# Kernel tuning notes

Measured on AMD Instinct MI355X. Metric: run time of the kernel, lower is better.

## Reference

```python
import jax, jax.numpy as jnp
import numpy as np

UNITS = 256
NUM_HEADS = 8
HEAD_DIM = UNITS // NUM_HEADS
B, N = 8, 2048


def setup_inputs() -> dict:
    key = jax.random.key(0)
    ks = jax.random.split(key, 7)
    node_features = jax.random.normal(ks[0], (B, N, UNITS), dtype=jnp.float32)
    adjacency_matrix = jax.random.randint(ks[1], (B, N, N), 0, 2, dtype=jnp.int32)
    # Glorot-ish scaled dense weights
    s = 1.0 / np.sqrt(UNITS)
    Wq = jax.random.normal(ks[2], (UNITS, UNITS), dtype=jnp.float32) * s
    Wk = jax.random.normal(ks[3], (UNITS, UNITS), dtype=jnp.float32) * s
    Wv = jax.random.normal(ks[4], (UNITS, UNITS), dtype=jnp.float32) * s
    Wo = jax.random.normal(ks[5], (UNITS, UNITS), dtype=jnp.float32) * s
    bo = jnp.zeros((UNITS,), dtype=jnp.float32)
    return {"node_features": node_features, "adjacency_matrix": adjacency_matrix,
            "Wq": Wq, "Wk": Wk, "Wv": Wv, "Wo": Wo, "bo": bo}


def reference(node_features, adjacency_matrix, Wq, Wk, Wv, Wo, bo):
    b, n, _ = node_features.shape
    h, d = NUM_HEADS, HEAD_DIM
    # projections -> [b, h, n, d]
    q = (node_features @ Wq).reshape(b, n, h, d).transpose(0, 2, 1, 3)
    k = (node_features @ Wk).reshape(b, n, h, d).transpose(0, 2, 1, 3)
    v = (node_features @ Wv).reshape(b, n, h, d).transpose(0, 2, 1, 3)
    scores = jnp.einsum('bhqd,bhkd->bhqk', q, k) / jnp.sqrt(jnp.float32(d))
    mask = adjacency_matrix[:, None, :, :] > 0  # [b,1,n,n] broadcasts over heads
    scores = jnp.where(mask, scores, jnp.float32(-1e9))
    w = jax.nn.softmax(scores, axis=-1)
    # dropout is identity at inference (training=None)
    ctx = jnp.einsum('bhqk,bhkd->bhqd', w, v)
    ctx = ctx.transpose(0, 2, 1, 3).reshape(b, n, h * d)
    return ctx @ Wo + bo
```

## Files before the change

kernel.cpp:

```cpp
#include <hip/hip_runtime.h>
#include <cstdint>
#include <cstddef>

#define B_ 8
#define N_ 2048
#define H_ 8
#define D_ 32
#define U_ 256

typedef _Float16 half8 __attribute__((ext_vector_type(8)));
typedef _Float16 half4 __attribute__((ext_vector_type(4)));
typedef float float4v __attribute__((ext_vector_type(4)));

__device__ __forceinline__ float fast_exp2(float x) {
#if __has_builtin(__builtin_amdgcn_exp2f)
  return __builtin_amdgcn_exp2f(x);
#else
  return exp2f(x);
#endif
}

__global__ __launch_bounds__(256, 2)
void k_qkv(const float* __restrict__ X,
           const float* __restrict__ Wq, const float* __restrict__ Wk,
           const float* __restrict__ Wv,
           _Float16* __restrict__ Qg, _Float16* __restrict__ Kg,
           _Float16* __restrict__ VTg)
{
  __shared__ __attribute__((aligned(16))) char qsmem[36864];
  _Float16* Xs = (_Float16*)qsmem;
  _Float16* Ws = (_Float16*)(qsmem + 18432);

  const int tid  = threadIdx.x;
  const int lane = tid & 63;
  const int w    = tid >> 6;
  const int c    = lane & 15;
  const int qd   = lane >> 4;

  const int bx   = blockIdx.x;
  const int proj = bx >> 1;
  const int nh   = bx & 1;
  const int n0l  = nh * 128;
  const int m0   = blockIdx.y * 128;
  const float* Wp = (proj == 0) ? Wq : ((proj == 1) ? Wk : Wv);
  const float wscale = (proj == 0) ? 0.25505413f : 1.0f;

  const float4v zero4 = {0.f, 0.f, 0.f, 0.f};
  float4v acc[2][8];
#pragma unroll
  for (int i = 0; i < 2; ++i)
#pragma unroll
    for (int j = 0; j < 8; ++j) acc[i][j] = zero4;

  for (int kt = 0; kt < 4; ++kt) {
    const int k0 = kt * 64;
    {
      const int row = tid >> 1;
      const int off = (tid & 1) * 32;
      const float* src = X + (size_t)(m0 + row) * U_ + k0 + off;
      _Float16* dst = &Xs[row * 72 + off];
#pragma unroll
      for (int i = 0; i < 4; ++i) {
        float4v a  = *(const float4v*)(src + i * 8);
        float4v b2 = *(const float4v*)(src + i * 8 + 4);
        half8 hv;
        hv[0] = (_Float16)a[0];  hv[1] = (_Float16)a[1];
        hv[2] = (_Float16)a[2];  hv[3] = (_Float16)a[3];
        hv[4] = (_Float16)b2[0]; hv[5] = (_Float16)b2[1];
        hv[6] = (_Float16)b2[2]; hv[7] = (_Float16)b2[3];
        *(half8*)(dst + i * 8) = hv;
      }
    }
    {
      const int kl = tid & 63;
      const int ng = tid >> 6;
      const float* srcw = Wp + (size_t)(k0 + kl) * U_ + n0l + ng * 32;
#pragma unroll
      for (int j = 0; j < 8; ++j) {
        float4v a = *(const float4v*)(srcw + j * 4);
#pragma unroll
        for (int jj = 0; jj < 4; ++jj)
          Ws[(ng * 32 + j * 4 + jj) * 72 + kl] = (_Float16)(a[jj] * wscale);
      }
    }
    __syncthreads();
#pragma unroll
    for (int ks = 0; ks < 2; ++ks) {
      half8 af[2], bf[8];
#pragma unroll
      for (int mt = 0; mt < 2; ++mt)
        af[mt] = *(const half8*)&Xs[(w * 32 + mt * 16 + c) * 72 + ks * 32 + qd * 8];
#pragma unroll
      for (int nt = 0; nt < 8; ++nt)
        bf[nt] = *(const half8*)&Ws[(nt * 16 + c) * 72 + ks * 32 + qd * 8];
#pragma unroll
      for (int mt = 0; mt < 2; ++mt)
#pragma unroll
        for (int nt = 0; nt < 8; ++nt)
          acc[mt][nt] = __builtin_amdgcn_mfma_f32_16x16x32_f16(af[mt], bf[nt], acc[mt][nt], 0, 0, 0);
    }
    __syncthreads();
  }

  const int b   = m0 >> 11;
  const int nb0 = m0 & (N_ - 1);
  if (proj < 2) {
    _Float16* Og = (proj == 0) ? Qg : Kg;
#pragma unroll
    for (int mt = 0; mt < 2; ++mt)
#pragma unroll
      for (int nt = 0; nt < 8; ++nt)
#pragma unroll
        for (int r = 0; r < 4; ++r) {
          const int rowl = w * 32 + mt * 16 + qd * 4 + r;
          Og[(size_t)(b * N_ + nb0 + rowl) * U_ + n0l + nt * 16 + c] = (_Float16)acc[mt][nt][r];
        }
  } else {
    _Float16* tr = (_Float16*)qsmem;
#pragma unroll
    for (int mt = 0; mt < 2; ++mt)
#pragma unroll
      for (int nt = 0; nt < 8; ++nt)
#pragma unroll
        for (int r = 0; r < 4; ++r)
          tr[(nt * 16 + c) * 136 + w * 32 + mt * 16 + qd * 4 + r] = (_Float16)acc[mt][nt][r];
    __syncthreads();
    const int u = tid >> 1;
    const int seg = tid & 1;
    _Float16* dst = VTg + (size_t)(b * U_ + n0l + u) * N_ + nb0 + seg * 64;
#pragma unroll
    for (int i = 0; i < 8; ++i)
      *(half8*)(dst + i * 8) = *(const half8*)&tr[u * 136 + seg * 64 + i * 8];
  }
}

#define KS_H (32 * 264)
#define VT_H (256 * 40)

struct StageRegs {
  half8 k0, k1, v0, v1;
  int a0, a1, a2, a3;
};

__global__ __launch_bounds__(512, 2)
void k_attn(const _Float16* __restrict__ Qg, const _Float16* __restrict__ Kg,
            const _Float16* __restrict__ VTg, const int* __restrict__ Adj,
            _Float16* __restrict__ Cg)
{
  __shared__ __attribute__((aligned(16))) _Float16 KsB[2][KS_H];
  __shared__ __attribute__((aligned(16))) _Float16 VTsB[2][VT_H];
  __shared__ __attribute__((aligned(8)))  unsigned int maskB[2][64];

  const int tid  = threadIdx.x;
  const int lane = tid & 63;
  const int w    = tid >> 6;
  const int c    = lane & 15;
  const int qd   = lane >> 4;
  const int wg   = blockIdx.x;
  const int b    = wg & 7;
  const int q0   = (wg >> 3) * 64;

  const _Float16* kptr = Kg + (size_t)(b * N_ + (tid >> 4)) * U_ + (tid & 15) * 16;
  const _Float16* vptr = VTg + (size_t)(b * U_ + (tid >> 1)) * N_ + (tid & 1) * 16;
  const int rr = lane >> 5;
  const int kk = lane & 31;
  const int* aptr = Adj + (size_t)(b * N_ + q0 + w * 8 + rr) * N_ + kk;

  half8 qb[4];
#pragma unroll
  for (int nt = 0; nt < 4; ++nt)
    qb[nt] = *(const half8*)(Qg + (size_t)(b * N_ + q0 + nt * 16 + c) * U_ + w * D_ + qd * 8);

  const float4v init4 = {-8.f, -8.f, -8.f, -8.f};
  const float4v zero4 = {0.f, 0.f, 0.f, 0.f};
  float4v acc[2][4];
#pragma unroll
  for (int i = 0; i < 2; ++i)
#pragma unroll
    for (int j = 0; j < 4; ++j) acc[i][j] = zero4;
  float lrow[4] = {0.f, 0.f, 0.f, 0.f};

  auto load_tile = [&](int kt) -> StageRegs {
    StageRegs r;
    const _Float16* ks = kptr + (size_t)kt * 32 * U_;
    const _Float16* vs = vptr + (size_t)kt * 32;
    const int* as = aptr + (size_t)kt * 32;
    r.k0 = *(const half8*)ks;  r.k1 = *(const half8*)(ks + 8);
    r.v0 = *(const half8*)vs;  r.v1 = *(const half8*)(vs + 8);
    r.a0 = as[0];
    r.a1 = as[2 * N_];
    r.a2 = as[4 * N_];
    r.a3 = as[6 * N_];
    return r;
  };
  auto store_tile = [&](const StageRegs& r, int buf) {
    _Float16* kd = &KsB[buf][(tid >> 4) * 264 + (tid & 15) * 16];
    *(half8*)kd = r.k0;  *(half8*)(kd + 8) = r.k1;
    _Float16* vd = &VTsB[buf][(tid >> 1) * 40 + (tid & 1) * 16];
    *(half8*)vd = r.v0;  *(half8*)(vd + 8) = r.v1;
    unsigned long long bm;
    bm = __ballot(r.a0 > 0); if (lane == 0) *(unsigned long long*)&maskB[buf][w * 8 + 0] = bm;
    bm = __ballot(r.a1 > 0); if (lane == 0) *(unsigned long long*)&maskB[buf][w * 8 + 2] = bm;
    bm = __ballot(r.a2 > 0); if (lane == 0) *(unsigned long long*)&maskB[buf][w * 8 + 4] = bm;
    bm = __ballot(r.a3 > 0); if (lane == 0) *(unsigned long long*)&maskB[buf][w * 8 + 6] = bm;
  };
  auto compute_tile = [&](int buf) {
    half8 ka0 = *(const half8*)&KsB[buf][(0 * 16 + c) * 264 + w * D_ + qd * 8];
    half8 ka1 = *(const half8*)&KsB[buf][(1 * 16 + c) * 264 + w * D_ + qd * 8];
    half4 va[2][2];
#pragma unroll
    for (int mt = 0; mt < 2; ++mt)
#pragma unroll
      for (int kc = 0; kc < 2; ++kc)
        va[mt][kc] = *(const half4*)&VTsB[buf][(w * D_ + mt * 16 + c) * 40 + kc * 16 + qd * 4];
#pragma unroll
    for (int nt = 0; nt < 4; ++nt) {
      float4v s0 = __builtin_amdgcn_mfma_f32_16x16x32_f16(ka0, qb[nt], init4, 0, 0, 0);
      float4v s1 = __builtin_amdgcn_mfma_f32_16x16x32_f16(ka1, qb[nt], init4, 0, 0, 0);
      const unsigned int mq = maskB[buf][nt * 16 + c];
      const unsigned int t0 = mq >> (qd * 4);
      const unsigned int t1 = mq >> (16 + qd * 4);
      half4 pb0, pb1;
      float ls = 0.f;
#pragma unroll
      for (int r = 0; r < 4; ++r) {
        float e0 = fast_exp2(s0[r]);
        float e1 = fast_exp2(s1[r]);
        float p0 = ((t0 >> r) & 1u) ? e0 : 0.f;
        float p1 = ((t1 >> r) & 1u) ? e1 : 0.f;
        ls += p0 + p1;
        pb0[r] = (_Float16)p0;
        pb1[r] = (_Float16)p1;
      }
      lrow[nt] += ls;
      acc[0][nt] = __builtin_amdgcn_mfma_f32_16x16x16f16(va[0][0], pb0, acc[0][nt], 0, 0, 0);
      acc[0][nt] = __builtin_amdgcn_mfma_f32_16x16x16f16(va[0][1], pb1, acc[0][nt], 0, 0, 0);
      acc[1][nt] = __builtin_amdgcn_mfma_f32_16x16x16f16(va[1][0], pb0, acc[1][nt], 0, 0, 0);
      acc[1][nt] = __builtin_amdgcn_mfma_f32_16x16x16f16(va[1][1], pb1, acc[1][nt], 0, 0, 0);
    }
  };

  {
    StageRegs r = load_tile(0);
    store_tile(r, 0);
  }
  __syncthreads();

#pragma unroll 1
  for (int kt = 0; kt < 64; kt += 2) {
    {
      StageRegs r = load_tile(kt + 1);
      compute_tile(0);
      store_tile(r, 1);
    }
    __syncthreads();
    if (kt + 2 < 64) {
      StageRegs r = load_tile(kt + 2);
      compute_tile(1);
      store_tile(r, 0);
    } else {
      compute_tile(1);
    }
    __syncthreads();
  }

  float rinv[4];
#pragma unroll
  for (int nt = 0; nt < 4; ++nt) {
    float l = lrow[nt];
    l += __shfl_xor(l, 16, 64);
    l += __shfl_xor(l, 32, 64);
    rinv[nt] = (l > 0.f) ? 1.f / l : 0.f;
  }
  _Float16* ctxS = (_Float16*)KsB;
#pragma unroll
  for (int mt = 0; mt < 2; ++mt)
#pragma unroll
    for (int nt = 0; nt < 4; ++nt) {
      half4 hv;
#pragma unroll
      for (int r = 0; r < 4; ++r)
        hv[r] = (_Float16)(acc[mt][nt][r] * rinv[nt]);
      *(half4*)&ctxS[(nt * 16 + c) * 264 + w * D_ + mt * 16 + qd * 4] = hv;
    }
  __syncthreads();
  {
    const int row = tid >> 3;
    const int seg = tid & 7;
    _Float16* dst = Cg + (size_t)(b * N_ + q0 + row) * U_ + seg * 32;
#pragma unroll
    for (int i = 0; i < 4; ++i)
      *(half8*)(dst + i * 8) = *(const half8*)&ctxS[row * 264 + seg * 32 + i * 8];
  }
}

__global__ __launch_bounds__(256, 2)
void k_out(const _Float16* __restrict__ Cg, const float* __restrict__ Wo,
           const float* __restrict__ bo, float* __restrict__ Out)
{
  __shared__ __attribute__((aligned(16))) char osmem[36864];
  _Float16* Xs = (_Float16*)osmem;
  _Float16* Ws = (_Float16*)(osmem + 18432);

  const int tid  = threadIdx.x;
  const int lane = tid & 63;
  const int w    = tid >> 6;
  const int c    = lane & 15;
  const int qd   = lane >> 4;
  const int n0l  = blockIdx.x * 128;
  const int m0   = blockIdx.y * 128;

  const float4v zero4 = {0.f, 0.f, 0.f, 0.f};
  float4v acc[2][8];
#pragma unroll
  for (int i = 0; i < 2; ++i)
#pragma unroll
    for (int j = 0; j < 8; ++j) acc[i][j] = zero4;

  for (int kt = 0; kt < 4; ++kt) {
    const int k0 = kt * 64;
    {
      const int row = tid >> 1;
      const int off = (tid & 1) * 32;
      const _Float16* src = Cg + (size_t)(m0 + row) * U_ + k0 + off;
      _Float16* dst = &Xs[row * 72 + off];
#pragma unroll
      for (int i = 0; i < 4; ++i)
        *(half8*)(dst + i * 8) = *(const half8*)(src + i * 8);
    }
    {
      const int kl = tid & 63;
      const int ng = tid >> 6;
      const float* srcw = Wo + (size_t)(k0 + kl) * U_ + n0l + ng * 32;
#pragma unroll
      for (int j = 0; j < 8; ++j) {
        float4v a = *(const float4v*)(srcw + j * 4);
#pragma unroll
        for (int jj = 0; jj < 4; ++jj)
          Ws[(ng * 32 + j * 4 + jj) * 72 + kl] = (_Float16)a[jj];
      }
    }
    __syncthreads();
#pragma unroll
    for (int ks = 0; ks < 2; ++ks) {
      half8 af[2], bf[8];
#pragma unroll
      for (int mt = 0; mt < 2; ++mt)
        af[mt] = *(const half8*)&Xs[(w * 32 + mt * 16 + c) * 72 + ks * 32 + qd * 8];
#pragma unroll
      for (int nt = 0; nt < 8; ++nt)
        bf[nt] = *(const half8*)&Ws[(nt * 16 + c) * 72 + ks * 32 + qd * 8];
#pragma unroll
      for (int mt = 0; mt < 2; ++mt)
#pragma unroll
        for (int nt = 0; nt < 8; ++nt)
          acc[mt][nt] = __builtin_amdgcn_mfma_f32_16x16x32_f16(af[mt], bf[nt], acc[mt][nt], 0, 0, 0);
    }
    __syncthreads();
  }

#pragma unroll
  for (int nt = 0; nt < 8; ++nt) {
    const float bias = bo[n0l + nt * 16 + c];
#pragma unroll
    for (int mt = 0; mt < 2; ++mt)
#pragma unroll
      for (int r = 0; r < 4; ++r) {
        const int rowl = w * 32 + mt * 16 + qd * 4 + r;
        Out[(size_t)(m0 + rowl) * U_ + n0l + nt * 16 + c] = acc[mt][nt][r] + bias;
      }
  }
}

extern "C" void kernel_launch(void* const* d_in, const int* in_sizes, int n_in,
                              void* d_out, int out_size, void* d_ws, size_t ws_size,
                              hipStream_t stream) {
  const float* X   = (const float*)d_in[0];
  const int*   Adj = (const int*)d_in[1];
  const float* Wq  = (const float*)d_in[2];
  const float* Wk  = (const float*)d_in[3];
  const float* Wv  = (const float*)d_in[4];
  const float* Wo  = (const float*)d_in[5];
  const float* bo  = (const float*)d_in[6];
  float* Out = (float*)d_out;

  const size_t elems = (size_t)B_ * N_ * U_;
  _Float16* Qg  = (_Float16*)d_ws;
  _Float16* Kg  = Qg + elems;
  _Float16* VTg = Kg + elems;
  _Float16* Cg  = VTg + elems;

  k_qkv<<<dim3(6, 128), 256, 0, stream>>>(X, Wq, Wk, Wv, Qg, Kg, VTg);
  k_attn<<<dim3(256), 512, 0, stream>>>(Qg, Kg, VTg, Adj, Cg);
  k_out<<<dim3(2, 128), 256, 0, stream>>>(Cg, Wo, bo, Out);
}
```

Baseline: 351.8 us.

## Prepack fp16 inputs/weights, drop LDS staging in GEMMs, halve attention query tile

```diff
diff --git a/kernel.cpp b/kernel.cpp
--- a/kernel.cpp
+++ b/kernel.cpp
@@ -20,30 +20,76 @@
 #endif
 }
 
+__global__ __launch_bounds__(256)
+void k_prep(const float* __restrict__ X,
+            const float* __restrict__ Wq, const float* __restrict__ Wk,
+            const float* __restrict__ Wv, const float* __restrict__ Wo,
+            _Float16* __restrict__ Xh, _Float16* __restrict__ WT)
+{
+  const int bid = blockIdx.x, tid = threadIdx.x;
+  if (bid < 512) {
+    const size_t base = ((size_t)bid * 256 + tid) * 32;
+    const float* src = X + base;
+    _Float16* dst = Xh + base;
+#pragma unroll
+    for (int i = 0; i < 4; ++i) {
+      float4v a = *(const float4v*)(src + i * 8);
+      float4v b = *(const float4v*)(src + i * 8 + 4);
+      half8 h;
+      h[0] = (_Float16)a[0]; h[1] = (_Float16)a[1];
+      h[2] = (_Float16)a[2]; h[3] = (_Float16)a[3];
+      h[4] = (_Float16)b[0]; h[5] = (_Float16)b[1];
+      h[6] = (_Float16)b[2]; h[7] = (_Float16)b[3];
+      *(half8*)(dst + i * 8) = h;
+    }
+  } else {
+    const int m = bid - 512;
+    const float* W = (m == 0) ? Wq : (m == 1) ? Wk : (m == 2) ? Wv : Wo;
+    const float scale = (m == 0) ? 0.25505413f : 1.0f;
+    _Float16* T = WT + (size_t)m * U_ * U_;
+    __shared__ _Float16 Ts[64][72];
+    const int r = tid >> 2, seg = tid & 3;
+    for (int t = 0; t < 16; ++t) {
+      const int k0 = (t >> 2) * 64, n0 = (t & 3) * 64;
+      float4v a[4];
+      const float* s = W + (size_t)(k0 + r) * U_ + n0 + seg * 16;
+#pragma unroll
+      for (int i = 0; i < 4; ++i) a[i] = *(const float4v*)(s + i * 4);
+      __syncthreads();
+#pragma unroll
+      for (int i = 0; i < 4; ++i)
+#pragma unroll
+        for (int j = 0; j < 4; ++j)
+          Ts[seg * 16 + i * 4 + j][r] = (_Float16)(a[i][j] * scale);
+      __syncthreads();
+      _Float16* d = T + (size_t)(n0 + r) * U_ + k0 + seg * 16;
+      *(half8*)d       = *(const half8*)&Ts[r][seg * 16];
+      *(half8*)(d + 8) = *(const half8*)&Ts[r][seg * 16 + 8];
+    }
+  }
+}
+
 __global__ __launch_bounds__(256, 2)
-void k_qkv(const float* __restrict__ X,
-           const float* __restrict__ Wq, const float* __restrict__ Wk,
-           const float* __restrict__ Wv,
+void k_qkv(const _Float16* __restrict__ Xh, const _Float16* __restrict__ WT,
            _Float16* __restrict__ Qg, _Float16* __restrict__ Kg,
            _Float16* __restrict__ VTg)
 {
-  __shared__ __attribute__((aligned(16))) char qsmem[36864];
-  _Float16* Xs = (_Float16*)qsmem;
-  _Float16* Ws = (_Float16*)(qsmem + 18432);
+  __shared__ __attribute__((aligned(16))) _Float16 tr[128 * 136];
 
   const int tid  = threadIdx.x;
   const int lane = tid & 63;
   const int w    = tid >> 6;
   const int c    = lane & 15;
   const int qd   = lane >> 4;
-
   const int bx   = blockIdx.x;
   const int proj = bx >> 1;
-  const int nh   = bx & 1;
-  const int n0l  = nh * 128;
+  const int n0l  = (bx & 1) * 128;
   const int m0   = blockIdx.y * 128;
-  const float* Wp = (proj == 0) ? Wq : ((proj == 1) ? Wk : Wv);
-  const float wscale = (proj == 0) ? 0.25505413f : 1.0f;
+
+  const _Float16* Wp = WT + (size_t)proj * U_ * U_;
+  const _Float16* arow0 = Xh + (size_t)(m0 + w * 32 + c) * U_ + qd * 8;
+  const _Float16* arow1 = arow0 + (size_t)16 * U_;
+  const _Float16* brow  = Wp + (size_t)(n0l + c) * U_ + qd * 8;
 
   const float4v zero4 = {0.f, 0.f, 0.f, 0.f};
   float4v acc[2][8];
@@ -52,54 +98,20 @@
 #pragma unroll
     for (int j = 0; j < 8; ++j) acc[i][j] = zero4;
 
-  for (int kt = 0; kt < 4; ++kt) {
-    const int k0 = kt * 64;
-    {
-      const int row = tid >> 1;
-      const int off = (tid & 1) * 32;
-      const float* src = X + (size_t)(m0 + row) * U_ + k0 + off;
-      _Float16* dst = &Xs[row * 72 + off];
-#pragma unroll
-      for (int i = 0; i < 4; ++i) {
-        float4v a  = *(const float4v*)(src + i * 8);
-        float4v b2 = *(const float4v*)(src + i * 8 + 4);
-        half8 hv;
-        hv[0] = (_Float16)a[0];  hv[1] = (_Float16)a[1];
-        hv[2] = (_Float16)a[2];  hv[3] = (_Float16)a[3];
-        hv[4] = (_Float16)b2[0]; hv[5] = (_Float16)b2[1];
-        hv[6] = (_Float16)b2[2]; hv[7] = (_Float16)b2[3];
-        *(half8*)(dst + i * 8) = hv;
-      }
-    }
-    {
-      const int kl = tid & 63;
-      const int ng = tid >> 6;
-      const float* srcw = Wp + (size_t)(k0 + kl) * U_ + n0l + ng * 32;
-#pragma unroll
-      for (int j = 0; j < 8; ++j) {
-        float4v a = *(const float4v*)(srcw + j * 4);
-#pragma unroll
-        for (int jj = 0; jj < 4; ++jj)
-          Ws[(ng * 32 + j * 4 + jj) * 72 + kl] = (_Float16)(a[jj] * wscale);
-      }
-    }
-    __syncthreads();
-#pragma unroll
-    for (int ks = 0; ks < 2; ++ks) {
-      half8 af[2], bf[8];
-#pragma unroll
-      for (int mt = 0; mt < 2; ++mt)
-        af[mt] = *(const half8*)&Xs[(w * 32 + mt * 16 + c) * 72 + ks * 32 + qd * 8];
-#pragma unroll
-      for (int nt = 0; nt < 8; ++nt)
-        bf[nt] = *(const half8*)&Ws[(nt * 16 + c) * 72 + ks * 32 + qd * 8];
-#pragma unroll
-      for (int mt = 0; mt < 2; ++mt)
-#pragma unroll
-        for (int nt = 0; nt < 8; ++nt)
-          acc[mt][nt] = __builtin_amdgcn_mfma_f32_16x16x32_f16(af[mt], bf[nt], acc[mt][nt], 0, 0, 0);
-    }
-    __syncthreads();
+#pragma unroll 2
+  for (int ks = 0; ks < 8; ++ks) {
+    const int k0 = ks * 32;
+    half8 af0 = *(const half8*)(arow0 + k0);
+    half8 af1 = *(const half8*)(arow1 + k0);
+    half8 bf[8];
+#pragma unroll
+    for (int nt = 0; nt < 8; ++nt)
+      bf[nt] = *(const half8*)(brow + (size_t)nt * 16 * U_ + k0);
+#pragma unroll
+    for (int nt = 0; nt < 8; ++nt) {
+      acc[0][nt] = __builtin_amdgcn_mfma_f32_16x16x32_f16(af0, bf[nt], acc[0][nt], 0, 0, 0);
+      acc[1][nt] = __builtin_amdgcn_mfma_f32_16x16x32_f16(af1, bf[nt], acc[1][nt], 0, 0, 0);
+    }
   }
 
   const int b   = m0 >> 11;
@@ -116,7 +128,6 @@
           Og[(size_t)(b * N_ + nb0 + rowl) * U_ + n0l + nt * 16 + c] = (_Float16)acc[mt][nt][r];
         }
   } else {
-    _Float16* tr = (_Float16*)qsmem;
 #pragma unroll
     for (int mt = 0; mt < 2; ++mt)
 #pragma unroll
@@ -139,7 +150,7 @@
 
 struct StageRegs {
   half8 k0, k1, v0, v1;
-  int a0, a1, a2, a3;
+  int a0, a1;
 };
 
 __global__ __launch_bounds__(512, 2)
@@ -149,7 +160,7 @@
 {
   __shared__ __attribute__((aligned(16))) _Float16 KsB[2][KS_H];
   __shared__ __attribute__((aligned(16))) _Float16 VTsB[2][VT_H];
-  __shared__ __attribute__((aligned(8)))  unsigned int maskB[2][64];
+  __shared__ __attribute__((aligned(8)))  unsigned int maskB[2][32];
 
   const int tid  = threadIdx.x;
   const int lane = tid & 63;
@@ -158,27 +169,27 @@
   const int qd   = lane >> 4;
   const int wg   = blockIdx.x;
   const int b    = wg & 7;
-  const int q0   = (wg >> 3) * 64;
+  const int q0   = (wg >> 3) * 32;
 
   const _Float16* kptr = Kg + (size_t)(b * N_ + (tid >> 4)) * U_ + (tid & 15) * 16;
   const _Float16* vptr = VTg + (size_t)(b * U_ + (tid >> 1)) * N_ + (tid & 1) * 16;
   const int rr = lane >> 5;
   const int kk = lane & 31;
-  const int* aptr = Adj + (size_t)(b * N_ + q0 + w * 8 + rr) * N_ + kk;
-
-  half8 qb[4];
-#pragma unroll
-  for (int nt = 0; nt < 4; ++nt)
+  const int* aptr = Adj + (size_t)(b * N_ + q0 + w * 4 + rr) * N_ + kk;
+
+  half8 qb[2];
+#pragma unroll
+  for (int nt = 0; nt < 2; ++nt)
     qb[nt] = *(const half8*)(Qg + (size_t)(b * N_ + q0 + nt * 16 + c) * U_ + w * D_ + qd * 8);
 
   const float4v init4 = {-8.f, -8.f, -8.f, -8.f};
   const float4v zero4 = {0.f, 0.f, 0.f, 0.f};
-  float4v acc[2][4];
+  float4v acc[2][2];
 #pragma unroll
   for (int i = 0; i < 2; ++i)
 #pragma unroll
-    for (int j = 0; j < 4; ++j) acc[i][j] = zero4;
-  float lrow[4] = {0.f, 0.f, 0.f, 0.f};
+    for (int j = 0; j < 2; ++j) acc[i][j] = zero4;
+  float lrow[2] = {0.f, 0.f};
 
   auto load_tile = [&](int kt) -> StageRegs {
     StageRegs r;
@@ -189,8 +200,6 @@
     r.v0 = *(const half8*)vs;  r.v1 = *(const half8*)(vs + 8);
     r.a0 = as[0];
     r.a1 = as[2 * N_];
-    r.a2 = as[4 * N_];
-    r.a3 = as[6 * N_];
     return r;
   };
   auto store_tile = [&](const StageRegs& r, int buf) {
@@ -199,10 +208,8 @@
     _Float16* vd = &VTsB[buf][(tid >> 1) * 40 + (tid & 1) * 16];
     *(half8*)vd = r.v0;  *(half8*)(vd + 8) = r.v1;
     unsigned long long bm;
-    bm = __ballot(r.a0 > 0); if (lane == 0) *(unsigned long long*)&maskB[buf][w * 8 + 0] = bm;
-    bm = __ballot(r.a1 > 0); if (lane == 0) *(unsigned long long*)&maskB[buf][w * 8 + 2] = bm;
-    bm = __ballot(r.a2 > 0); if (lane == 0) *(unsigned long long*)&maskB[buf][w * 8 + 4] = bm;
-    bm = __ballot(r.a3 > 0); if (lane == 0) *(unsigned long long*)&maskB[buf][w * 8 + 6] = bm;
+    bm = __ballot(r.a0 > 0); if (lane == 0) *(unsigned long long*)&maskB[buf][w * 4 + 0] = bm;
+    bm = __ballot(r.a1 > 0); if (lane == 0) *(unsigned long long*)&maskB[buf][w * 4 + 2] = bm;
   };
   auto compute_tile = [&](int buf) {
     half8 ka0 = *(const half8*)&KsB[buf][(0 * 16 + c) * 264 + w * D_ + qd * 8];
@@ -214,7 +221,7 @@
       for (int kc = 0; kc < 2; ++kc)
         va[mt][kc] = *(const half4*)&VTsB[buf][(w * D_ + mt * 16 + c) * 40 + kc * 16 + qd * 4];
 #pragma unroll
-    for (int nt = 0; nt < 4; ++nt) {
+    for (int nt = 0; nt < 2; ++nt) {
       float4v s0 = __builtin_amdgcn_mfma_f32_16x16x32_f16(ka0, qb[nt], init4, 0, 0, 0);
       float4v s1 = __builtin_amdgcn_mfma_f32_16x16x32_f16(ka1, qb[nt], init4, 0, 0, 0);
       const unsigned int mq = maskB[buf][nt * 16 + c];
@@ -264,9 +271,9 @@
     __syncthreads();
   }
 
-  float rinv[4];
-#pragma unroll
-  for (int nt = 0; nt < 4; ++nt) {
+  float rinv[2];
+#pragma unroll
+  for (int nt = 0; nt < 2; ++nt) {
     float l = lrow[nt];
     l += __shfl_xor(l, 16, 64);
     l += __shfl_xor(l, 32, 64);
@@ -276,7 +283,7 @@
 #pragma unroll
   for (int mt = 0; mt < 2; ++mt)
 #pragma unroll
-    for (int nt = 0; nt < 4; ++nt) {
+    for (int nt = 0; nt < 2; ++nt) {
       half4 hv;
 #pragma unroll
       for (int r = 0; r < 4; ++r)
@@ -285,23 +292,18 @@
     }
   __syncthreads();
   {
-    const int row = tid >> 3;
-    const int seg = tid & 7;
-    _Float16* dst = Cg + (size_t)(b * N_ + q0 + row) * U_ + seg * 32;
-#pragma unroll
-    for (int i = 0; i < 4; ++i)
-      *(half8*)(dst + i * 8) = *(const half8*)&ctxS[row * 264 + seg * 32 + i * 8];
+    const int row = tid >> 4;
+    const int seg = tid & 15;
+    _Float16* dst = Cg + (size_t)(b * N_ + q0 + row) * U_ + seg * 16;
+    *(half8*)dst       = *(const half8*)&ctxS[row * 264 + seg * 16];
+    *(half8*)(dst + 8) = *(const half8*)&ctxS[row * 264 + seg * 16 + 8];
   }
 }
 
 __global__ __launch_bounds__(256, 2)
-void k_out(const _Float16* __restrict__ Cg, const float* __restrict__ Wo,
+void k_out(const _Float16* __restrict__ Cg, const _Float16* __restrict__ WTo,
            const float* __restrict__ bo, float* __restrict__ Out)
 {
-  __shared__ __attribute__((aligned(16))) char osmem[36864];
-  _Float16* Xs = (_Float16*)osmem;
-  _Float16* Ws = (_Float16*)(osmem + 18432);
-
   const int tid  = threadIdx.x;
   const int lane = tid & 63;
   const int w    = tid >> 6;
@@ -310,6 +312,10 @@
   const int n0l  = blockIdx.x * 128;
   const int m0   = blockIdx.y * 128;
 
+  const _Float16* arow0 = Cg + (size_t)(m0 + w * 32 + c) * U_ + qd * 8;
+  const _Float16* arow1 = arow0 + (size_t)16 * U_;
+  const _Float16* brow  = WTo + (size_t)(n0l + c) * U_ + qd * 8;
+
   const float4v zero4 = {0.f, 0.f, 0.f, 0.f};
   float4v acc[2][8];
 #pragma unroll
@@ -317,46 +323,20 @@
 #pragma unroll
     for (int j = 0; j < 8; ++j) acc[i][j] = zero4;
 
-  for (int kt = 0; kt < 4; ++kt) {
-    const int k0 = kt * 64;
-    {
-      const int row = tid >> 1;
-      const int off = (tid & 1) * 32;
-      const _Float16* src = Cg + (size_t)(m0 + row) * U_ + k0 + off;
-      _Float16* dst = &Xs[row * 72 + off];
-#pragma unroll
-      for (int i = 0; i < 4; ++i)
-        *(half8*)(dst + i * 8) = *(const half8*)(src + i * 8);
-    }
-    {
-      const int kl = tid & 63;
-      const int ng = tid >> 6;
-      const float* srcw = Wo + (size_t)(k0 + kl) * U_ + n0l + ng * 32;
-#pragma unroll
-      for (int j = 0; j < 8; ++j) {
-        float4v a = *(const float4v*)(srcw + j * 4);
-#pragma unroll
-        for (int jj = 0; jj < 4; ++jj)
-          Ws[(ng * 32 + j * 4 + jj) * 72 + kl] = (_Float16)a[jj];
-      }
-    }
-    __syncthreads();
-#pragma unroll
-    for (int ks = 0; ks < 2; ++ks) {
-      half8 af[2], bf[8];
-#pragma unroll
-      for (int mt = 0; mt < 2; ++mt)
-        af[mt] = *(const half8*)&Xs[(w * 32 + mt * 16 + c) * 72 + ks * 32 + qd * 8];
-#pragma unroll
-      for (int nt = 0; nt < 8; ++nt)
-        bf[nt] = *(const half8*)&Ws[(nt * 16 + c) * 72 + ks * 32 + qd * 8];
-#pragma unroll
-      for (int mt = 0; mt < 2; ++mt)
-#pragma unroll
-        for (int nt = 0; nt < 8; ++nt)
-          acc[mt][nt] = __builtin_amdgcn_mfma_f32_16x16x32_f16(af[mt], bf[nt], acc[mt][nt], 0, 0, 0);
-    }
-    __syncthreads();
+#pragma unroll 2
+  for (int ks = 0; ks < 8; ++ks) {
+    const int k0 = ks * 32;
+    half8 af0 = *(const half8*)(arow0 + k0);
+    half8 af1 = *(const half8*)(arow1 + k0);
+    half8 bf[8];
+#pragma unroll
+    for (int nt = 0; nt < 8; ++nt)
+      bf[nt] = *(const half8*)(brow + (size_t)nt * 16 * U_ + k0);
+#pragma unroll
+    for (int nt = 0; nt < 8; ++nt) {
+      acc[0][nt] = __builtin_amdgcn_mfma_f32_16x16x32_f16(af0, bf[nt], acc[0][nt], 0, 0, 0);
+      acc[1][nt] = __builtin_amdgcn_mfma_f32_16x16x32_f16(af1, bf[nt], acc[1][nt], 0, 0, 0);
+    }
   }
 
 #pragma unroll
@@ -388,9 +368,12 @@
   _Float16* Qg  = (_Float16*)d_ws;
   _Float16* Kg  = Qg + elems;
   _Float16* VTg = Kg + elems;
-  _Float16* Cg  = VTg + elems;
-
-  k_qkv<<<dim3(6, 128), 256, 0, stream>>>(X, Wq, Wk, Wv, Qg, Kg, VTg);
-  k_attn<<<dim3(256), 512, 0, stream>>>(Qg, Kg, VTg, Adj, Cg);
-  k_out<<<dim3(2, 128), 256, 0, stream>>>(Cg, Wo, bo, Out);
-}
+  _Float16* Xh  = VTg + elems;
+  _Float16* Cg  = Xh;
+  _Float16* WT  = Xh + elems;
+
+  k_prep<<<dim3(516), 256, 0, stream>>>(X, Wq, Wk, Wv, Wo, Xh, WT);
+  k_qkv<<<dim3(6, 128), 256, 0, stream>>>(Xh, WT, Qg, Kg, VTg);
+  k_attn<<<dim3(512), 512, 0, stream>>>(Qg, Kg, VTg, Adj, Cg);
+  k_out<<<dim3(2, 128), 256, 0, stream>>>(Cg, WT + 3 * U_ * U_, bo, Out);
+}
```

Result: slower. 361.5 us (+2.8%).
